# Performance work log

Hardware: AMD Instinct MI355X
Metric: run time of the kernel (lower is better)

## Reference

```python
import jax, jax.numpy as jnp
import numpy as np

N, CH, H, W = 8, 256, 64, 64
M, K = 4, 256
CG = CH // M  # per-group input channels


def setup_inputs() -> dict:
    key = jax.random.key(0)
    k1, k2 = jax.random.split(key)
    x = jax.random.normal(k1, (N, CH, H, W), dtype=jnp.float32)
    # grouped conv1x1 weight: [m, k, c_g]  (torch layout is [m*k, c_g, 1, 1])
    w = jax.random.normal(k2, (M, K, CG), dtype=jnp.float32) / np.float32(np.sqrt(CG))
    return {"x": x, "w": w}


def reference(x, w):
    n, c, h, wd = x.shape
    m, k, cg = w.shape
    # grouped 1x1 conv == per-group matmul over channels
    xg = x.reshape(n, m, cg, h, wd)
    logit5 = jnp.einsum('nmchw,mkc->nmhwk', xg, w)  # [n, m, h, w, k]
    # OneHotCategoricalStraightThrough.rsample():
    # hard one-hot sample + (probs - stop_grad(probs))
    probs = jax.nn.softmax(logit5, axis=-1)
    idx = jax.random.categorical(jax.random.key(42), logit5, axis=-1)  # [n, m, h, w]
    one_hot = jax.nn.one_hot(idx, k, dtype=logit5.dtype)
    quantized = jax.lax.stop_gradient(one_hot) + probs - jax.lax.stop_gradient(probs)
    code = jnp.argmax(quantized, axis=-1)  # [n, m, h, w]
    q_out = jnp.transpose(quantized, (0, 1, 4, 2, 3)).reshape(n, m * k, h, wd)
    logit = jnp.transpose(logit5, (0, 1, 4, 2, 3)).reshape(n, m * k, h, wd)
    return q_out, code, logit
```

## Files before the change

### kernel.cpp

```cpp
#include <hip/hip_runtime.h>
#include <stdint.h>

#define CODE_OFF  33554432u
#define LOGIT_OFF 33685504u

typedef __attribute__((address_space(1))) const void g_void;
typedef __attribute__((address_space(3))) void l_void;

__device__ __forceinline__ uint32_t rotl32(uint32_t x, int r) {
  return (x << r) | (x >> (32 - r));
}

__device__ __forceinline__ uint32_t tf32_part(uint32_t i) {
  const uint32_t ks1 = 42u;
  const uint32_t ks2 = 0x1BD11BDAu ^ 42u;
  uint32_t x0 = 0u;
  uint32_t x1 = i + ks1;
#define R4(a,b,c,d) \
  x0 += x1; x1 = rotl32(x1,(a)); x1 ^= x0; \
  x0 += x1; x1 = rotl32(x1,(b)); x1 ^= x0; \
  x0 += x1; x1 = rotl32(x1,(c)); x1 ^= x0; \
  x0 += x1; x1 = rotl32(x1,(d)); x1 ^= x0;
  R4(13,15,26,6)   x0 += ks1; x1 += ks2 + 1u;
  R4(17,29,16,24)  x0 += ks2; x1 += 2u;
  R4(13,15,26,6)               x1 += ks1 + 3u;
  R4(17,29,16,24)  x0 += ks1; x1 += ks2 + 4u;
  R4(13,15,26,6)   x0 += ks2; x1 += 5u;
#undef R4
  return x0 ^ x1;
}

__device__ __forceinline__ float bits_to_gumbel(uint32_t bits) {
  uint32_t fb = (bits >> 9) | 0x3f800000u;
  float f = __uint_as_float(fb) - 1.0f;
  float u = (f > 0.0f) ? f : 1.17549435e-38f;
  return -logf(-logf(u));
}

__global__ __launch_bounds__(256, 4)
void mcq_kernel(const float* __restrict__ x, const float* __restrict__ w,
                float* __restrict__ out) {
  __shared__ __align__(16) float x_lds[2048];
  __shared__ __align__(16) float w_lds[2048];

  const int tid = threadIdx.x;
  const int tx = tid & 7;
  const int ty = tid >> 3;
  const int half = tx >> 2;
  const int px = tx & 3;
  const int bid = blockIdx.x;
  const int nm = bid >> 8;
  const int tile = bid & 255;
  const int hw0 = tile * 16;
  const int n = nm >> 2;
  const int m = nm & 3;

  float* q_out = out;
  float* code_out = out + CODE_OFF;
  float* logit_out = out + LOGIT_OFF;

  {
    const float* xA = x + (size_t)(n * 256 + m * 64) * 4096 + hw0;
    const float* xB = xA + (size_t)4 * 256 * 4096;
#pragma unroll
    for (int it = 0; it < 2; ++it) {
      int idx = it * 256 + tid;
      int c = idx >> 3;
      int hs = (idx >> 2) & 1;
      int ck = idx & 3;
      const float* src = (hs ? xB : xA) + (size_t)c * 4096 + ck * 4;
      float* dst = x_lds + ((it * 256 + (tid & ~63)) << 2);
      __builtin_amdgcn_global_load_lds((g_void*)src, (l_void*)dst, 16, 0, 0);
    }
  }

  const float* wrow = w + (size_t)m * 256 * 64;
  float4 wr0, wr1;
  {
    const float* wk = wrow + tid * 64;
    wr0 = *(const float4*)(wk + 0);
    wr1 = *(const float4*)(wk + 4);
    w_lds[0 * 256 + tid] = wr0.x; w_lds[1 * 256 + tid] = wr0.y;
    w_lds[2 * 256 + tid] = wr0.z; w_lds[3 * 256 + tid] = wr0.w;
    w_lds[4 * 256 + tid] = wr1.x; w_lds[5 * 256 + tid] = wr1.y;
    w_lds[6 * 256 + tid] = wr1.z; w_lds[7 * 256 + tid] = wr1.w;
  }
  __syncthreads();

  float acc0[8], acc1[8], acc2[8], acc3[8];
#pragma unroll
  for (int i = 0; i < 8; ++i) acc0[i] = acc1[i] = acc2[i] = acc3[i] = 0.0f;

#pragma unroll
  for (int chunk = 0; chunk < 8; ++chunk) {
    if (chunk < 7) {
      const float* wk = wrow + tid * 64 + (chunk + 1) * 8;
      wr0 = *(const float4*)(wk + 0);
      wr1 = *(const float4*)(wk + 4);
    }
#pragma unroll
    for (int cc = 0; cc < 8; ++cc) {
      int c = chunk * 8 + cc;
      float4 xv = *(const float4*)&x_lds[c * 32 + half * 16 + px * 4];
      float wv[8];
      *(float4*)&wv[0] = *(const float4*)&w_lds[cc * 256 +   0 + ty * 4];
      *(float4*)&wv[4] = *(const float4*)&w_lds[cc * 256 + 128 + ty * 4];
#pragma unroll
      for (int jd = 0; jd < 8; ++jd) {
        float wkv = wv[jd];
        acc0[jd] += xv.x * wkv;
        acc1[jd] += xv.y * wkv;
        acc2[jd] += xv.z * wkv;
        acc3[jd] += xv.w * wkv;
      }
    }
    if (chunk < 7) {
      __syncthreads();
      w_lds[0 * 256 + tid] = wr0.x; w_lds[1 * 256 + tid] = wr0.y;
      w_lds[2 * 256 + tid] = wr0.z; w_lds[3 * 256 + tid] = wr0.w;
      w_lds[4 * 256 + tid] = wr1.x; w_lds[5 * 256 + tid] = wr1.y;
      w_lds[6 * 256 + tid] = wr1.z; w_lds[7 * 256 + tid] = wr1.w;
      __syncthreads();
    }
  }

  float best0 = -3.4e38f, best1 = -3.4e38f, best2 = -3.4e38f, best3 = -3.4e38f;
  int i0 = 0, i1 = 0, i2 = 0, i3 = 0;
  const uint32_t base0 = ((uint32_t)((nm + 16 * half) * 4096 + hw0 + 4 * px)) << 8;
  const size_t row_off = (size_t)hw0 + 4 * px;
#pragma unroll
  for (int jd = 0; jd < 8; ++jd) {
    int k = (jd >> 2) * 128 + ty * 4 + (jd & 3);
    size_t off = (size_t)((nm + 16 * half) * 256 + k) * 4096 + row_off;
    *(float4*)(logit_out + off) = make_float4(acc0[jd], acc1[jd], acc2[jd], acc3[jd]);
    uint32_t b0 = tf32_part(base0 + 0u * 256u + (uint32_t)k);
    uint32_t b1 = tf32_part(base0 + 1u * 256u + (uint32_t)k);
    uint32_t b2 = tf32_part(base0 + 2u * 256u + (uint32_t)k);
    uint32_t b3 = tf32_part(base0 + 3u * 256u + (uint32_t)k);
    float v0 = bits_to_gumbel(b0) + acc0[jd];
    float v1 = bits_to_gumbel(b1) + acc1[jd];
    float v2 = bits_to_gumbel(b2) + acc2[jd];
    float v3 = bits_to_gumbel(b3) + acc3[jd];
    if (v0 > best0) { best0 = v0; i0 = k; }
    if (v1 > best1) { best1 = v1; i1 = k; }
    if (v2 > best2) { best2 = v2; i2 = k; }
    if (v3 > best3) { best3 = v3; i3 = k; }
  }

  __syncthreads();
  float* red_val = x_lds;
  int* red_idx = (int*)w_lds;
  {
    int slot = half * 16 + px * 4;
    red_val[(slot + 0) * 33 + ty] = best0;  red_idx[(slot + 0) * 33 + ty] = i0;
    red_val[(slot + 1) * 33 + ty] = best1;  red_idx[(slot + 1) * 33 + ty] = i1;
    red_val[(slot + 2) * 33 + ty] = best2;  red_idx[(slot + 2) * 33 + ty] = i2;
    red_val[(slot + 3) * 33 + ty] = best3;  red_idx[(slot + 3) * 33 + ty] = i3;
  }
  __syncthreads();
  int* idx_final = (int*)(x_lds + 1088);
  if (tid < 32) {
    float bv = -3.4e38f; int bi = 0x7fffffff;
#pragma unroll
    for (int t2 = 0; t2 < 32; ++t2) {
      float v = red_val[tid * 33 + t2];
      int ix = red_idx[tid * 33 + t2];
      if (v > bv || (v == bv && ix < bi)) { bv = v; bi = ix; }
    }
    idx_final[tid] = bi;
    int h = tid >> 4;
    int pos = tid & 15;
    code_out[(size_t)(nm + 16 * h) * 4096 + hw0 + pos] = (float)bi;
  }
  __syncthreads();

  const int f0 = idx_final[half * 16 + px * 4 + 0];
  const int f1 = idx_final[half * 16 + px * 4 + 1];
  const int f2 = idx_final[half * 16 + px * 4 + 2];
  const int f3 = idx_final[half * 16 + px * 4 + 3];
#pragma unroll
  for (int jd = 0; jd < 8; ++jd) {
    int k = (jd >> 2) * 128 + ty * 4 + (jd & 3);
    size_t off = (size_t)((nm + 16 * half) * 256 + k) * 4096 + row_off;
    *(float4*)(q_out + off) = make_float4(k == f0 ? 1.0f : 0.0f, k == f1 ? 1.0f : 0.0f,
                                          k == f2 ? 1.0f : 0.0f, k == f3 ? 1.0f : 0.0f);
  }
}

extern "C" void kernel_launch(void* const* d_in, const int* in_sizes, int n_in,
                              void* d_out, int out_size, void* d_ws, size_t ws_size,
                              hipStream_t stream) {
  const float* x = (const float*)d_in[0];
  const float* w = (const float*)d_in[1];
  float* out = (float*)d_out;
  mcq_kernel<<<dim3(4096), dim3(256), 0, stream>>>(x, w, out);
}
```

Measured before the change: 397.5 us.

## Interleave Gumbel noise generation with matmul and double-buffer weight LDS

Computes the Threefry-based Gumbel noise for each k column inside the channel-chunk loop, so the integer hash and log work can overlap with the FMA/LDS matmul instead of running serially afterwards. The weight tile in LDS is double-buffered, which drops one barrier per chunk. This adds 32 live floats per thread and doubles the weight LDS footprint, which risks register spills or reduced occupancy.

Measured after the change: 382.7 us. 1.04x faster.

```diff
diff --git a/kernel.cpp b/kernel.cpp
--- a/kernel.cpp
+++ b/kernel.cpp
@@ -41,7 +41,7 @@
 void mcq_kernel(const float* __restrict__ x, const float* __restrict__ w,
                 float* __restrict__ out) {
   __shared__ __align__(16) float x_lds[2048];
-  __shared__ __align__(16) float w_lds[2048];
+  __shared__ __align__(16) float w_lds[4096];
 
   const int tid = threadIdx.x;
   const int tx = tid & 7;
@@ -88,8 +88,11 @@
   __syncthreads();
 
   float acc0[8], acc1[8], acc2[8], acc3[8];
+  float gmb0[8], gmb1[8], gmb2[8], gmb3[8];
 #pragma unroll
   for (int i = 0; i < 8; ++i) acc0[i] = acc1[i] = acc2[i] = acc3[i] = 0.0f;
+
+  const uint32_t base0 = ((uint32_t)((nm + 16 * half) * 4096 + hw0 + 4 * px)) << 8;
 
 #pragma unroll
   for (int chunk = 0; chunk < 8; ++chunk) {
@@ -98,13 +101,25 @@
       wr0 = *(const float4*)(wk + 0);
       wr1 = *(const float4*)(wk + 4);
     }
+    {
+      const uint32_t k = (uint32_t)((chunk >> 2) * 128 + ty * 4 + (chunk & 3));
+      uint32_t b0 = tf32_part(base0 + 0u * 256u + k);
+      uint32_t b1 = tf32_part(base0 + 1u * 256u + k);
+      uint32_t b2 = tf32_part(base0 + 2u * 256u + k);
+      uint32_t b3 = tf32_part(base0 + 3u * 256u + k);
+      gmb0[chunk] = bits_to_gumbel(b0);
+      gmb1[chunk] = bits_to_gumbel(b1);
+      gmb2[chunk] = bits_to_gumbel(b2);
+      gmb3[chunk] = bits_to_gumbel(b3);
+    }
+    const int rb = (chunk & 1) * 2048;
 #pragma unroll
     for (int cc = 0; cc < 8; ++cc) {
       int c = chunk * 8 + cc;
       float4 xv = *(const float4*)&x_lds[c * 32 + half * 16 + px * 4];
       float wv[8];
-      *(float4*)&wv[0] = *(const float4*)&w_lds[cc * 256 +   0 + ty * 4];
-      *(float4*)&wv[4] = *(const float4*)&w_lds[cc * 256 + 128 + ty * 4];
+      *(float4*)&wv[0] = *(const float4*)&w_lds[rb + cc * 256 +   0 + ty * 4];
+      *(float4*)&wv[4] = *(const float4*)&w_lds[rb + cc * 256 + 128 + ty * 4];
 #pragma unroll
       for (int jd = 0; jd < 8; ++jd) {
         float wkv = wv[jd];
@@ -115,32 +130,27 @@
       }
     }
     if (chunk < 7) {
-      __syncthreads();
-      w_lds[0 * 256 + tid] = wr0.x; w_lds[1 * 256 + tid] = wr0.y;
-      w_lds[2 * 256 + tid] = wr0.z; w_lds[3 * 256 + tid] = wr0.w;
-      w_lds[4 * 256 + tid] = wr1.x; w_lds[5 * 256 + tid] = wr1.y;
-      w_lds[6 * 256 + tid] = wr1.z; w_lds[7 * 256 + tid] = wr1.w;
+      const int wb = ((chunk + 1) & 1) * 2048;
+      w_lds[wb + 0 * 256 + tid] = wr0.x; w_lds[wb + 1 * 256 + tid] = wr0.y;
+      w_lds[wb + 2 * 256 + tid] = wr0.z; w_lds[wb + 3 * 256 + tid] = wr0.w;
+      w_lds[wb + 4 * 256 + tid] = wr1.x; w_lds[wb + 5 * 256 + tid] = wr1.y;
+      w_lds[wb + 6 * 256 + tid] = wr1.z; w_lds[wb + 7 * 256 + tid] = wr1.w;
       __syncthreads();
     }
   }
 
   float best0 = -3.4e38f, best1 = -3.4e38f, best2 = -3.4e38f, best3 = -3.4e38f;
   int i0 = 0, i1 = 0, i2 = 0, i3 = 0;
-  const uint32_t base0 = ((uint32_t)((nm + 16 * half) * 4096 + hw0 + 4 * px)) << 8;
   const size_t row_off = (size_t)hw0 + 4 * px;
 #pragma unroll
   for (int jd = 0; jd < 8; ++jd) {
     int k = (jd >> 2) * 128 + ty * 4 + (jd & 3);
     size_t off = (size_t)((nm + 16 * half) * 256 + k) * 4096 + row_off;
     *(float4*)(logit_out + off) = make_float4(acc0[jd], acc1[jd], acc2[jd], acc3[jd]);
-    uint32_t b0 = tf32_part(base0 + 0u * 256u + (uint32_t)k);
-    uint32_t b1 = tf32_part(base0 + 1u * 256u + (uint32_t)k);
-    uint32_t b2 = tf32_part(base0 + 2u * 256u + (uint32_t)k);
-    uint32_t b3 = tf32_part(base0 + 3u * 256u + (uint32_t)k);
-    float v0 = bits_to_gumbel(b0) + acc0[jd];
-    float v1 = bits_to_gumbel(b1) + acc1[jd];
-    float v2 = bits_to_gumbel(b2) + acc2[jd];
-    float v3 = bits_to_gumbel(b3) + acc3[jd];
+    float v0 = gmb0[jd] + acc0[jd];
+    float v1 = gmb1[jd] + acc1[jd];
+    float v2 = gmb2[jd] + acc2[jd];
+    float v3 = gmb3[jd] + acc3[jd];
     if (v0 > best0) { best0 = v0; i0 = k; }
     if (v1 > best1) { best1 = v1; i1 = k; }
     if (v2 > best2) { best2 = v2; i2 = k; }
```
